# Performance work log

Hardware: AMD Instinct MI355X
Metric: run time of the kernel (lower is better)

The kernel has to match this reference:

```python
import jax, jax.numpy as jnp
import numpy as np

B, L, E, Q = 32, 2048, 512, 512

def setup_inputs() -> dict:
    key = jax.random.key(0)
    k1, k2, k3, k4, k5 = jax.random.split(key, 5)
    scale_attn = 1.0 / np.sqrt(E + Q)
    scale_v = 1.0 / np.sqrt(E)
    return {
        "embeddings": jax.random.normal(k1, (B, L, E), dtype=jnp.float32),
        "query": jax.random.normal(k2, (B, L, Q), dtype=jnp.float32),
        "W_attn": jax.random.normal(k3, (E, E + Q), dtype=jnp.float32) * scale_attn,
        "b_attn": jax.random.normal(k4, (E,), dtype=jnp.float32) * scale_attn,
        "v_w": jax.random.normal(k5, (E,), dtype=jnp.float32) * scale_v,
    }

def reference(embeddings, query, W_attn, b_attn, v_w):
    # concat along feature dim: (B, L, Q+E)
    cat = jnp.concatenate([query, embeddings], axis=2)
    # attn_layer: Linear(E+Q -> E), then tanh: (B, L, E)
    h = jnp.tanh(jnp.einsum('blf,ef->ble', cat, W_attn) + b_attn)
    # attn_v: Linear(E -> 1, no bias) -> scores (B, L)
    scores = jnp.einsum('ble,e->bl', h, v_w)
    # softmax over the sequence (dim=1 in torch)
    w = jax.nn.softmax(scores, axis=1)  # (B, L)
    # transpose to (B, 1, L) then bmm with embeddings -> (B, 1, E)
    applied = jnp.einsum('bl,ble->be', w, embeddings)[:, None, :]
    weights = w[:, None, :]
    return (applied, weights)
```

## Files before the change

### kernel.cpp

```cpp
#include <hip/hip_runtime.h>
#include <hip/hip_bf16.h>
#include <math.h>


typedef __attribute__((ext_vector_type(8))) short bf16x8;
typedef __attribute__((ext_vector_type(4))) float f32x4;

#define BDIM 32
#define LDIM 2048
#define EDIM 512
#define QDIM 512
#define KDIM 1024
#define MDIM (BDIM * LDIM)

#define BM 128
#define BN 128
#define BK 64
#define LDS_STRIDE (BK + 8)

__device__ inline unsigned int pack2bf(float lo, float hi) {
    unsigned int a = __builtin_bit_cast(unsigned int, lo) + 0x8000u;
    unsigned int b = __builtin_bit_cast(unsigned int, hi) + 0x8000u;
    return __builtin_amdgcn_perm(b, a, 0x07060302);
}

__global__ __launch_bounds__(256) void scores_kernel(
    const float* __restrict__ emb, const float* __restrict__ query,
    const float* __restrict__ W, const float* __restrict__ b_attn,
    const float* __restrict__ v_w, float* __restrict__ scores)
{
    __shared__ unsigned short As[BM][LDS_STRIDE];
    __shared__ unsigned short Bs[BN][LDS_STRIDE];

    const int tid = threadIdx.x;
    const int bid = blockIdx.x;
    const int xcd = bid & 7;
    const int slot = bid >> 3;
    const int mtile = xcd * 64 + (slot >> 2);
    const int ntile = slot & 3;
    const int m0 = mtile * BM;
    const int n0 = ntile * BN;

    const int lane = tid & 63;
    const int wv = tid >> 6;
    const int wm = (wv >> 1) * 64;
    const int wn = (wv & 1) * 64;
    const int quad = lane >> 4;
    const int ln = lane & 15;

    const int row16 = tid >> 4;
    const int col4  = (tid & 15) * 4;

    f32x4 acc[4][4];
    #pragma unroll
    for (int i = 0; i < 4; i++)
        #pragma unroll
        for (int j = 0; j < 4; j++)
            acc[i][j] = (f32x4){0.f, 0.f, 0.f, 0.f};

    for (int k0 = 0; k0 < KDIM; k0 += BK) {
        const float* asrc = (k0 < QDIM) ? query : emb;
        const int koff = (k0 < QDIM) ? k0 : (k0 - QDIM);
        #pragma unroll
        for (int p = 0; p < 8; p++) {
            const int r = p * 16 + row16;
            const float4 v = *(const float4*)(asrc + (size_t)(m0 + r) * 512 + koff + col4);
            uint2 pk;
            pk.x = pack2bf(v.x, v.y);
            pk.y = pack2bf(v.z, v.w);
            *(uint2*)&As[r][col4] = pk;
        }
        #pragma unroll
        for (int p = 0; p < 8; p++) {
            const int r = p * 16 + row16;
            const float4 v = *(const float4*)(W + (size_t)(n0 + r) * 1024 + k0 + col4);
            uint2 pk;
            pk.x = pack2bf(v.x, v.y);
            pk.y = pack2bf(v.z, v.w);
            *(uint2*)&Bs[r][col4] = pk;
        }
        __syncthreads();

        #pragma unroll
        for (int ks = 0; ks < 2; ks++) {
            bf16x8 af[4], bf[4];
            #pragma unroll
            for (int i = 0; i < 4; i++)
                af[i] = *(const bf16x8*)&As[wm + i * 16 + ln][ks * 32 + quad * 8];
            #pragma unroll
            for (int j = 0; j < 4; j++)
                bf[j] = *(const bf16x8*)&Bs[wn + j * 16 + ln][ks * 32 + quad * 8];
            #pragma unroll
            for (int i = 0; i < 4; i++)
                #pragma unroll
                for (int j = 0; j < 4; j++)
                    acc[i][j] = __builtin_amdgcn_mfma_f32_16x16x32_bf16(af[i], bf[j], acc[i][j], 0, 0, 0);
        }
        __syncthreads();
    }

    float bj[4], vj[4];
    #pragma unroll
    for (int j = 0; j < 4; j++) {
        const int n = n0 + wn + j * 16 + ln;
        bj[j] = b_attn[n];
        vj[j] = v_w[n];
    }
    #pragma unroll
    for (int i = 0; i < 4; i++) {
        #pragma unroll
        for (int r = 0; r < 4; r++) {
            float s = 0.f;
            #pragma unroll
            for (int j = 0; j < 4; j++)
                s += tanhf(acc[i][j][r] + bj[j]) * vj[j];
            #pragma unroll
            for (int off = 1; off < 16; off <<= 1)
                s += __shfl_xor(s, off, 64);
            if (ln == 0)
                atomicAdd(&scores[m0 + wm + i * 16 + quad * 4 + r], s);
        }
    }
}

__global__ __launch_bounds__(256) void softmax_apply_kernel(
    const float* __restrict__ emb, const float* __restrict__ scores,
    float* __restrict__ out_applied, float* __restrict__ out_weights)
{
    const int b = blockIdx.x >> 5;
    const int chunk = blockIdx.x & 31;
    const int l0 = chunk * 64;
    const int tid = threadIdx.x;
    const float* srow = scores + b * LDIM;

    __shared__ float red[4];
    __shared__ float wls[64];
    __shared__ float partial[128 * 4];

    float mx = -1e30f;
    #pragma unroll
    for (int t = 0; t < 8; t++) mx = fmaxf(mx, srow[tid + t * 256]);
    #pragma unroll
    for (int off = 1; off < 64; off <<= 1) mx = fmaxf(mx, __shfl_xor(mx, off, 64));
    if ((tid & 63) == 0) red[tid >> 6] = mx;
    __syncthreads();
    mx = fmaxf(fmaxf(red[0], red[1]), fmaxf(red[2], red[3]));

    float sm = 0.f;
    #pragma unroll
    for (int t = 0; t < 8; t++) sm += expf(srow[tid + t * 256] - mx);
    #pragma unroll
    for (int off = 1; off < 64; off <<= 1) sm += __shfl_xor(sm, off, 64);
    __syncthreads();
    if ((tid & 63) == 0) red[tid >> 6] = sm;
    __syncthreads();
    sm = red[0] + red[1] + red[2] + red[3];
    const float inv = 1.f / sm;

    if (tid < 64) {
        const float w = expf(srow[l0 + tid] - mx) * inv;
        wls[tid] = w;
        out_weights[(size_t)b * LDIM + l0 + tid] = w;
    }
    __syncthreads();

    const int half = tid >> 7;
    const int cg = tid & 127;
    float4 acc = {0.f, 0.f, 0.f, 0.f};
    const float* ebase = emb + ((size_t)b * LDIM + l0 + half) * EDIM + cg * 4;
    #pragma unroll 8
    for (int i = 0; i < 32; i++) {
        const float4 v = *(const float4*)(ebase + (size_t)2 * i * EDIM);
        const float w = wls[half + 2 * i];
        acc.x += w * v.x;
        acc.y += w * v.y;
        acc.z += w * v.z;
        acc.w += w * v.w;
    }
    if (half == 1) *(float4*)&partial[cg * 4] = acc;
    __syncthreads();
    if (half == 0) {
        const float4 p = *(const float4*)&partial[cg * 4];
        float* dst = out_applied + b * EDIM + cg * 4;
        atomicAdd(dst + 0, acc.x + p.x);
        atomicAdd(dst + 1, acc.y + p.y);
        atomicAdd(dst + 2, acc.z + p.z);
        atomicAdd(dst + 3, acc.w + p.w);
    }
}

extern "C" void kernel_launch(void* const* d_in, const int* in_sizes, int n_in,
                              void* d_out, int out_size, void* d_ws, size_t ws_size,
                              hipStream_t stream) {
    const float* emb    = (const float*)d_in[0];
    const float* query  = (const float*)d_in[1];
    const float* W      = (const float*)d_in[2];
    const float* b_attn = (const float*)d_in[3];
    const float* v_w    = (const float*)d_in[4];

    float* out     = (float*)d_out;
    float* applied = out;
    float* weights = out + BDIM * EDIM;
    float* scores  = (float*)d_ws;

    hipMemsetAsync(scores, 0, (size_t)MDIM * sizeof(float), stream);
    hipMemsetAsync(applied, 0, (size_t)BDIM * EDIM * sizeof(float), stream);

    scores_kernel<<<2048, 256, 0, stream>>>(emb, query, W, b_attn, v_w, scores);

    softmax_apply_kernel<<<1024, 256, 0, stream>>>(emb, scores, applied, weights);
}
```

Baseline: 406.2 us.

## Prefetch next K-tile into registers, use exp-based tanh and RNE bf16 packing

The GEMM loop now loads the next K-slice of activations and weights into registers while the current slice's MFMAs run, giving a software pipeline over global loads. The epilogue replaces tanhf with an __expf-based tanh, and the bf16 conversion switches from a rounding bit trick to the HIP RNE intrinsic. Register-prefetching doubles the staging registers (32 float4), which may lower occupancy or cause spills. The exp-based tanh is less accurate for large |x|.

```diff
diff --git a/kernel.cpp b/kernel.cpp
--- a/kernel.cpp
+++ b/kernel.cpp
@@ -18,10 +18,16 @@
 #define BK 64
 #define LDS_STRIDE (BK + 8)
 
-__device__ inline unsigned int pack2bf(float lo, float hi) {
-    unsigned int a = __builtin_bit_cast(unsigned int, lo) + 0x8000u;
-    unsigned int b = __builtin_bit_cast(unsigned int, hi) + 0x8000u;
-    return __builtin_amdgcn_perm(b, a, 0x07060302);
+__device__ inline unsigned int pack2(float lo, float hi) {
+    __hip_bfloat162 h = __float22bfloat162_rn(float2{lo, hi});
+    unsigned int u;
+    __builtin_memcpy(&u, &h, sizeof(u));
+    return u;
+}
+
+__device__ inline float fast_tanh(float x) {
+    float e = __expf(2.0f * x);
+    return 1.0f - 2.0f / (e + 1.0f);
 }
 
 __global__ __launch_bounds__(256) void scores_kernel(
@@ -58,28 +64,44 @@
         for (int j = 0; j < 4; j++)
             acc[i][j] = (f32x4){0.f, 0.f, 0.f, 0.f};
 
+    float4 ra[8], rb[8], na[8], nb[8];
+
+    #pragma unroll
+    for (int p = 0; p < 8; p++)
+        ra[p] = *(const float4*)(query + (size_t)(m0 + p * 16 + row16) * 512 + col4);
+    #pragma unroll
+    for (int p = 0; p < 8; p++)
+        rb[p] = *(const float4*)(W + (size_t)(n0 + p * 16 + row16) * 1024 + col4);
+
+    #pragma unroll 2
     for (int k0 = 0; k0 < KDIM; k0 += BK) {
-        const float* asrc = (k0 < QDIM) ? query : emb;
-        const int koff = (k0 < QDIM) ? k0 : (k0 - QDIM);
         #pragma unroll
         for (int p = 0; p < 8; p++) {
-            const int r = p * 16 + row16;
-            const float4 v = *(const float4*)(asrc + (size_t)(m0 + r) * 512 + koff + col4);
             uint2 pk;
-            pk.x = pack2bf(v.x, v.y);
-            pk.y = pack2bf(v.z, v.w);
-            *(uint2*)&As[r][col4] = pk;
+            pk.x = pack2(ra[p].x, ra[p].y);
+            pk.y = pack2(ra[p].z, ra[p].w);
+            *(uint2*)&As[p * 16 + row16][col4] = pk;
         }
         #pragma unroll
         for (int p = 0; p < 8; p++) {
-            const int r = p * 16 + row16;
-            const float4 v = *(const float4*)(W + (size_t)(n0 + r) * 1024 + k0 + col4);
             uint2 pk;
-            pk.x = pack2bf(v.x, v.y);
-            pk.y = pack2bf(v.z, v.w);
-            *(uint2*)&Bs[r][col4] = pk;
+            pk.x = pack2(rb[p].x, rb[p].y);
+            pk.y = pack2(rb[p].z, rb[p].w);
+            *(uint2*)&Bs[p * 16 + row16][col4] = pk;
         }
         __syncthreads();
+
+        const int k1 = k0 + BK;
+        if (k1 < KDIM) {
+            const float* asrc = (k1 < QDIM) ? query : emb;
+            const int koff = k1 & (QDIM - 1);
+            #pragma unroll
+            for (int p = 0; p < 8; p++)
+                na[p] = *(const float4*)(asrc + (size_t)(m0 + p * 16 + row16) * 512 + koff + col4);
+            #pragma unroll
+            for (int p = 0; p < 8; p++)
+                nb[p] = *(const float4*)(W + (size_t)(n0 + p * 16 + row16) * 1024 + k1 + col4);
+        }
 
         #pragma unroll
         for (int ks = 0; ks < 2; ks++) {
@@ -97,6 +119,9 @@
                     acc[i][j] = __builtin_amdgcn_mfma_f32_16x16x32_bf16(af[i], bf[j], acc[i][j], 0, 0, 0);
         }
         __syncthreads();
+
+        #pragma unroll
+        for (int p = 0; p < 8; p++) { ra[p] = na[p]; rb[p] = nb[p]; }
     }
 
     float bj[4], vj[4];
@@ -113,7 +138,7 @@
             float s = 0.f;
             #pragma unroll
             for (int j = 0; j < 4; j++)
-                s += tanhf(acc[i][j][r] + bj[j]) * vj[j];
+                s += fast_tanh(acc[i][j][r] + bj[j]) * vj[j];
             #pragma unroll
             for (int off = 1; off < 16; off <<= 1)
                 s += __shfl_xor(s, off, 64);
@@ -203,8 +228,8 @@
     float* weights = out + BDIM * EDIM;
     float* scores  = (float*)d_ws;
 
-    hipMemsetAsync(scores, 0, (size_t)MDIM * sizeof(float), stream);
-    hipMemsetAsync(applied, 0, (size_t)BDIM * EDIM * sizeof(float), stream);
+    (void)hipMemsetAsync(scores, 0, (size_t)MDIM * sizeof(float), stream);
+    (void)hipMemsetAsync(applied, 0, (size_t)BDIM * EDIM * sizeof(float), stream);
 
     scores_kernel<<<2048, 256, 0, stream>>>(emb, query, W, b_attn, v_w, scores);
 
```

Result: slower. 498.0 us (+22.6%).
